# Kernel tuning notes

Measured on AMD Instinct MI355X. Metric: run time of the kernel, lower is better.

Reference implementation:

```python
import jax, jax.numpy as jnp
import numpy as np

HID = 128
N_BATCH = 16384


def gru_cell(x, h, Wih, Whh, bih, bhh):
    # PyTorch GRUCell: weight_ih [3H, in], weight_hh [3H, H], gate order r,z,n
    gi = x @ Wih.T + bih            # [N, 3H]
    gh = h @ Whh.T + bhh            # [N, 3H]
    ir, iz, ic = jnp.split(gi, 3, axis=-1)
    hr, hz, hc = jnp.split(gh, 3, axis=-1)
    r = jax.nn.sigmoid(ir + hr)
    z = jax.nn.sigmoid(iz + hz)
    c = jnp.tanh(ic + r * hc)
    return (1.0 - z) * c + z * h


def setup_inputs() -> dict:
    key = jax.random.key(0)
    ks = jax.random.split(key, 11)
    s = 0.05  # small init like uniform(-1/sqrt(H), 1/sqrt(H))
    return {
        "x": jax.random.normal(ks[0], (N_BATCH, 1, 28, 28), jnp.float32),
        "Wih1": jax.random.normal(ks[1], (3 * HID, 28), jnp.float32) * s,
        "Whh1": jax.random.normal(ks[2], (3 * HID, HID), jnp.float32) * s,
        "bih1": jax.random.normal(ks[3], (3 * HID,), jnp.float32) * s,
        "bhh1": jax.random.normal(ks[4], (3 * HID,), jnp.float32) * s,
        "Wih2": jax.random.normal(ks[5], (3 * HID, HID), jnp.float32) * s,
        "Whh2": jax.random.normal(ks[6], (3 * HID, HID), jnp.float32) * s,
        "bih2": jax.random.normal(ks[7], (3 * HID,), jnp.float32) * s,
        "bhh2": jax.random.normal(ks[8], (3 * HID,), jnp.float32) * s,
        "Wout": jax.random.normal(ks[9], (10, HID), jnp.float32) * s,
        "bout": jax.random.normal(ks[10], (10,), jnp.float32) * s,
    }


def reference(x, Wih1, Whh1, bih1, bhh1, Wih2, Whh2, bih2, bhh2, Wout, bout):
    n, c, h, w = x.shape
    xs = x.transpose(0, 2, 1, 3).reshape(n, h, w * c)  # [N, T=28, 28]
    xs = jnp.swapaxes(xs, 0, 1)                        # [T, N, 28]
    h1_0 = jnp.zeros((n, HID), x.dtype)
    zeros_h = jnp.zeros((n, HID), x.dtype)  # cell2 gets a fresh zero hidden each step (bug in source, kept)

    def step(h1, xt):
        h0 = jax.nn.relu(gru_cell(xt, h1, Wih1, Whh1, bih1, bhh1))
        h1_new = gru_cell(h0, zeros_h, Wih2, Whh2, bih2, bhh2)
        return h1_new, None

    h1, _ = jax.lax.scan(step, h1_0, xs)
    return h1 @ Wout.T + bout  # [N, 10]
```

## Files before the change

### kernel.cpp

```cpp
#include <hip/hip_runtime.h>
#include <hip/hip_bf16.h>
#include <stdint.h>

#define HID 128
#define NB 16384
#define TSTEPS 28
#define BN 64

typedef __attribute__((ext_vector_type(8))) short s16x8;
typedef __attribute__((ext_vector_type(4))) float f32x4;

#define H1_OFF 0
#define H0_OFF 17408
#define XT_OFF 34816
#define WI2_OFF 45056
#define SMEM_BYTES 143360
#define HSTRIDE 272
#define RFSTRIDE 4352
#define XSTRIDE 80

#define L2E 1.442695041f
#define TL2E 2.885390082f

__device__ __forceinline__ unsigned cvtpk2(float lo, float hi) {
  unsigned r;
  asm("v_cvt_pk_bf16_f32 %0, %1, %2" : "=v"(r) : "v"(lo), "v"(hi));
  return r;
}
__device__ __forceinline__ float sig_pre(float acc, float nb) {
  float e = __builtin_amdgcn_exp2f(fmaf(acc, -L2E, nb));
  return __builtin_amdgcn_rcpf(1.0f + e);
}
__device__ __forceinline__ float tanh_nc(float x) {
  float e2 = __builtin_amdgcn_exp2f(x * TL2E);
  float q = __builtin_amdgcn_rcpf(1.0f + e2);
  return fmaf(-2.0f, q, 1.0f);
}

__global__ __launch_bounds__(1024, 1) void gru_kernel(
    const float* __restrict__ x,
    const float* __restrict__ Wih1, const float* __restrict__ Whh1,
    const float* __restrict__ bih1, const float* __restrict__ bhh1,
    const float* __restrict__ Wih2,
    const float* __restrict__ bih2, const float* __restrict__ bhh2,
    const float* __restrict__ Wout, const float* __restrict__ bout,
    float* __restrict__ out)
{
  __shared__ char smem[SMEM_BYTES];
  const int tid = threadIdx.x;
  const int wv16 = tid >> 6;
  const int mh   = wv16 >> 3;
  const int cw   = wv16 & 7;
  const int lane = tid & 63;
  const int l15 = lane & 15;
  const int l16 = lane >> 4;
  const int hc0 = cw * 16;
  const int n0 = blockIdx.x * BN;

  f32x4 zq = {0.f, 0.f, 0.f, 0.f};
  asm("" : "+v"(zq));

  const int hrd = (mh * 32 + l15) * HSTRIDE + l16 * 16;
  const int hwr = (mh * 32 + 4 * l16) * HSTRIDE + (hc0 + l15) * 2;
  const int srow = tid >> 4, skp = tid & 15;
  const int xrd = XT_OFF + (mh * 32 + l15) * XSTRIDE + l16 * 16;
  const int xwr = XT_OFF + srow * XSTRIDE + skp * 4;
  const int wib = WI2_OFF + cw * 12288 + lane * 16;

  s16x8 fw_hh1[4][3];
  s16x8 fw_ih1[3];
  const int gb0 = hc0, gb1 = 128 + hc0, gb2 = 256 + hc0;
  #pragma unroll
  for (int kf = 0; kf < 4; ++kf) {
    int kbase = kf * 32 + l16 * 8;
    #pragma unroll
    for (int cb = 0; cb < 3; ++cb) {
      int g = (cb == 0 ? gb0 : cb == 1 ? gb1 : gb2) + l15;
      const float* p1 = Whh1 + g * HID + kbase;
      s16x8 f1;
      #pragma unroll
      for (int j = 0; j < 8; j += 2) {
        unsigned u1 = cvtpk2(p1[j], p1[j + 1]);
        f1[j] = (short)u1; f1[j + 1] = (short)(u1 >> 16);
      }
      fw_hh1[kf][cb] = f1;
      if (mh == 0) {
        const float* p2 = Wih2 + g * HID + kbase;
        s16x8 f2;
        #pragma unroll
        for (int j = 0; j < 8; j += 2) {
          unsigned u2 = cvtpk2(p2[j], p2[j + 1]);
          f2[j] = (short)u2; f2[j + 1] = (short)(u2 >> 16);
        }
        *(s16x8*)(smem + wib + (kf * 3 + cb) * 1024) = f2;
      }
    }
  }
  {
    int kbase = l16 * 8;
    #pragma unroll
    for (int cb = 0; cb < 3; ++cb) {
      int g = (cb == 0 ? gb0 : cb == 1 ? gb1 : gb2) + l15;
      s16x8 f;
      #pragma unroll
      for (int j = 0; j < 8; ++j) {
        int k = kbase + j;
        f[j] = (k < 28) ? (short)cvtpk2(Wih1[g * 28 + k], 0.f) : (short)0;
      }
      fw_ih1[cb] = f;
    }
  }
  const float nb_r  = -L2E * (bih1[gb0 + l15] + bhh1[gb0 + l15]);
  const float nb_z  = -L2E * (bih1[gb1 + l15] + bhh1[gb1 + l15]);
  const float b_ci  = bih1[gb2 + l15];
  const float b_ch  = bhh1[gb2 + l15];
  const float nb_r2 = -L2E * (bih2[gb0 + l15] + bhh2[gb0 + l15]);
  const float nb_z2 = -L2E * (bih2[gb1 + l15] + bhh2[gb1 + l15]);
  const float c_c2  = bih2[gb2 + l15];
  const float c_hc2 = bhh2[gb2 + l15];

  float h1reg[2][4];
  #pragma unroll
  for (int rf = 0; rf < 2; ++rf)
    #pragma unroll
    for (int j = 0; j < 4; ++j) h1reg[rf][j] = 0.f;

  const float2* xp0 = (const float2*)(x + (size_t)(n0 + srow) * 784 + 2 * skp);

  {
    float2 v0 = make_float2(0.f, 0.f);
    if (skp < 14) v0 = *xp0;
    xp0 += 14;
    *(unsigned*)(smem + xwr) = cvtpk2(v0.x, v0.y);
  }
  ((int4*)(smem + H1_OFF))[tid] = make_int4(0, 0, 0, 0);
  if (tid < 64) ((int4*)(smem + H1_OFF))[tid + 1024] = make_int4(0, 0, 0, 0);
  __syncthreads();

  #pragma unroll 1
  for (int t = 0; t < TSTEPS; ++t) {
    const int xb = (t & 1) * 5120;
    #pragma unroll
    for (int rf = 0; rf < 2; ++rf) {
      s16x8 ax = *(const s16x8*)(smem + xrd + xb + rf * 1280);
      f32x4 aR, aZ, aCi, aCh;
      aR  = __builtin_amdgcn_mfma_f32_16x16x32_bf16(ax, fw_ih1[0], zq, 0, 0, 0);
      aZ  = __builtin_amdgcn_mfma_f32_16x16x32_bf16(ax, fw_ih1[1], zq, 0, 0, 0);
      aCi = __builtin_amdgcn_mfma_f32_16x16x32_bf16(ax, fw_ih1[2], zq, 0, 0, 0);
      #pragma unroll
      for (int kf = 0; kf < 4; ++kf) {
        s16x8 ah = *(const s16x8*)(smem + H1_OFF + hrd + rf * RFSTRIDE + kf * 64);
        aR = __builtin_amdgcn_mfma_f32_16x16x32_bf16(ah, fw_hh1[kf][0], aR, 0, 0, 0);
        aZ = __builtin_amdgcn_mfma_f32_16x16x32_bf16(ah, fw_hh1[kf][1], aZ, 0, 0, 0);
        aCh = (kf == 0)
            ? __builtin_amdgcn_mfma_f32_16x16x32_bf16(ah, fw_hh1[0][2], zq, 0, 0, 0)
            : __builtin_amdgcn_mfma_f32_16x16x32_bf16(ah, fw_hh1[kf][2], aCh, 0, 0, 0);
      }
      float h0v[4];
      #pragma unroll
      for (int j = 0; j < 4; ++j) {
        float r = sig_pre(aR[j], nb_r);
        float z = sig_pre(aZ[j], nb_z);
        float c = tanh_nc(fmaf(r, aCh[j] + b_ch, aCi[j] + b_ci));
        h0v[j] = fmaxf(fmaf(z, h1reg[rf][j] - c, c), 0.f);
      }
      unsigned pk01 = cvtpk2(h0v[0], h0v[1]);
      unsigned pk23 = cvtpk2(h0v[2], h0v[3]);
      *(short*)(smem + H0_OFF + hwr + rf * RFSTRIDE + 0 * HSTRIDE) = (short)pk01;
      *(short*)(smem + H0_OFF + hwr + rf * RFSTRIDE + 1 * HSTRIDE) = (short)(pk01 >> 16);
      *(short*)(smem + H0_OFF + hwr + rf * RFSTRIDE + 2 * HSTRIDE) = (short)pk23;
      *(short*)(smem + H0_OFF + hwr + rf * RFSTRIDE + 3 * HSTRIDE) = (short)(pk23 >> 16);
    }
    __syncthreads();

    float2 xv0 = make_float2(0.f, 0.f);
    const bool do_stage = (t + 1 < TSTEPS);
    if (do_stage && skp < 14) xv0 = *xp0;
    xp0 += 14;
    #pragma unroll
    for (int p = 0; p < 2; ++p) {
      f32x4 aR2, aZ2, aC2;
      #pragma unroll
      for (int kf = 0; kf < 4; ++kf) {
        s16x8 a0 = *(const s16x8*)(smem + H0_OFF + hrd + p * RFSTRIDE + kf * 64);
        s16x8 b0 = *(const s16x8*)(smem + wib + (kf * 3 + 0) * 1024);
        s16x8 b1 = *(const s16x8*)(smem + wib + (kf * 3 + 1) * 1024);
        s16x8 b2 = *(const s16x8*)(smem + wib + (kf * 3 + 2) * 1024);
        if (kf == 0) {
          aR2 = __builtin_amdgcn_mfma_f32_16x16x32_bf16(a0, b0, zq, 0, 0, 0);
          aZ2 = __builtin_amdgcn_mfma_f32_16x16x32_bf16(a0, b1, zq, 0, 0, 0);
          aC2 = __builtin_amdgcn_mfma_f32_16x16x32_bf16(a0, b2, zq, 0, 0, 0);
        } else {
          aR2 = __builtin_amdgcn_mfma_f32_16x16x32_bf16(a0, b0, aR2, 0, 0, 0);
          aZ2 = __builtin_amdgcn_mfma_f32_16x16x32_bf16(a0, b1, aZ2, 0, 0, 0);
          aC2 = __builtin_amdgcn_mfma_f32_16x16x32_bf16(a0, b2, aC2, 0, 0, 0);
        }
      }
      float hv[4];
      #pragma unroll
      for (int j = 0; j < 4; ++j) {
        float r2 = sig_pre(aR2[j], nb_r2);
        float z2 = sig_pre(aZ2[j], nb_z2);
        float c2 = tanh_nc(fmaf(r2, c_hc2, aC2[j] + c_c2));
        float h1n = fmaf(-z2, c2, c2);
        h1reg[p][j] = h1n;
        hv[j] = h1n;
      }
      unsigned pk01 = cvtpk2(hv[0], hv[1]);
      unsigned pk23 = cvtpk2(hv[2], hv[3]);
      *(short*)(smem + H1_OFF + hwr + p * RFSTRIDE + 0 * HSTRIDE) = (short)pk01;
      *(short*)(smem + H1_OFF + hwr + p * RFSTRIDE + 1 * HSTRIDE) = (short)(pk01 >> 16);
      *(short*)(smem + H1_OFF + hwr + p * RFSTRIDE + 2 * HSTRIDE) = (short)pk23;
      *(short*)(smem + H1_OFF + hwr + p * RFSTRIDE + 3 * HSTRIDE) = (short)(pk23 >> 16);
    }
    if (do_stage) {
      const int xo = 5120 - xb;
      *(unsigned*)(smem + xwr + xo) = cvtpk2(xv0.x, xv0.y);
    }
    __syncthreads();
  }

  float* houtf = (float*)smem;
  #pragma unroll
  for (int rf = 0; rf < 2; ++rf)
    #pragma unroll
    for (int j = 0; j < 4; ++j) {
      int row = mh * 32 + rf * 16 + l16 * 4 + j;
      houtf[row * 132 + hc0 + l15] = h1reg[rf][j];
    }
  __syncthreads();
  if (tid < BN * 10) {
    int row = tid & 63;
    int o = tid >> 6;
    const float* hp = houtf + row * 132;
    const float* wp = Wout + o * HID;
    float s = bout[o];
    #pragma unroll 8
    for (int j2 = 0; j2 < HID; ++j2) s = fmaf(hp[j2], wp[j2], s);
    out[(size_t)(n0 + row) * 10 + o] = s;
  }
}

extern "C" void kernel_launch(void* const* d_in, const int* in_sizes, int n_in,
                              void* d_out, int out_size, void* d_ws, size_t ws_size,
                              hipStream_t stream) {
  const float* x    = (const float*)d_in[0];
  const float* Wih1 = (const float*)d_in[1];
  const float* Whh1 = (const float*)d_in[2];
  const float* bih1 = (const float*)d_in[3];
  const float* bhh1 = (const float*)d_in[4];
  const float* Wih2 = (const float*)d_in[5];
  const float* bih2 = (const float*)d_in[7];
  const float* bhh2 = (const float*)d_in[8];
  const float* Wout = (const float*)d_in[9];
  const float* bout = (const float*)d_in[10];
  gru_kernel<<<NB / BN, 1024, 0, stream>>>(x, Wih1, Whh1, bih1, bhh1,
                                           Wih2, bih2, bhh2, Wout, bout,
                                           (float*)d_out);
}
```

Before: 148.0 us.

## Halve block size, move Wih2 fragments to global workspace via prep kernel

```diff
diff --git a/kernel.cpp b/kernel.cpp
--- a/kernel.cpp
+++ b/kernel.cpp
@@ -5,16 +5,15 @@
 #define HID 128
 #define NB 16384
 #define TSTEPS 28
-#define BN 64
+#define BN 32
 
 typedef __attribute__((ext_vector_type(8))) short s16x8;
 typedef __attribute__((ext_vector_type(4))) float f32x4;
 
 #define H1_OFF 0
-#define H0_OFF 17408
-#define XT_OFF 34816
-#define WI2_OFF 45056
-#define SMEM_BYTES 143360
+#define H0_OFF 8704
+#define XT_OFF 17408
+#define SMEM_BYTES 22528
 #define HSTRIDE 272
 #define RFSTRIDE 4352
 #define XSTRIDE 80
@@ -37,20 +36,33 @@
   return fmaf(-2.0f, q, 1.0f);
 }
 
-__global__ __launch_bounds__(1024, 1) void gru_kernel(
+__global__ void prep_wih2(const float* __restrict__ Wih2, char* __restrict__ ws) {
+  const int b = blockIdx.x;
+  const int lane = threadIdx.x;
+  const int cb = b % 3, kf = (b / 3) & 3, cw = b / 12;
+  const int g = cb * 128 + cw * 16 + (lane & 15);
+  const float* p = Wih2 + g * HID + kf * 32 + (lane >> 4) * 8;
+  s16x8 f;
+  #pragma unroll
+  for (int j = 0; j < 8; j += 2) {
+    unsigned u = cvtpk2(p[j], p[j + 1]);
+    f[j] = (short)u; f[j + 1] = (short)(u >> 16);
+  }
+  *(s16x8*)(ws + (b * 64 + lane) * 16) = f;
+}
+
+__global__ __launch_bounds__(512, 4) void gru_kernel(
     const float* __restrict__ x,
     const float* __restrict__ Wih1, const float* __restrict__ Whh1,
     const float* __restrict__ bih1, const float* __restrict__ bhh1,
-    const float* __restrict__ Wih2,
+    const char* __restrict__ wfrag,
     const float* __restrict__ bih2, const float* __restrict__ bhh2,
     const float* __restrict__ Wout, const float* __restrict__ bout,
     float* __restrict__ out)
 {
   __shared__ char smem[SMEM_BYTES];
   const int tid = threadIdx.x;
-  const int wv16 = tid >> 6;
-  const int mh   = wv16 >> 3;
-  const int cw   = wv16 & 7;
+  const int cw   = tid >> 6;
   const int lane = tid & 63;
   const int l15 = lane & 15;
   const int l16 = lane >> 4;
@@ -60,12 +72,12 @@
   f32x4 zq = {0.f, 0.f, 0.f, 0.f};
   asm("" : "+v"(zq));
 
-  const int hrd = (mh * 32 + l15) * HSTRIDE + l16 * 16;
-  const int hwr = (mh * 32 + 4 * l16) * HSTRIDE + (hc0 + l15) * 2;
+  const int hrd = l15 * HSTRIDE + l16 * 16;
+  const int hwr = (4 * l16) * HSTRIDE + (hc0 + l15) * 2;
   const int srow = tid >> 4, skp = tid & 15;
-  const int xrd = XT_OFF + (mh * 32 + l15) * XSTRIDE + l16 * 16;
+  const int xrd = XT_OFF + l15 * XSTRIDE + l16 * 16;
   const int xwr = XT_OFF + srow * XSTRIDE + skp * 4;
-  const int wib = WI2_OFF + cw * 12288 + lane * 16;
+  const char* wsb = wfrag + cw * 12288 + lane * 16;
 
   s16x8 fw_hh1[4][3];
   s16x8 fw_ih1[3];
@@ -84,16 +96,6 @@
         f1[j] = (short)u1; f1[j + 1] = (short)(u1 >> 16);
       }
       fw_hh1[kf][cb] = f1;
-      if (mh == 0) {
-        const float* p2 = Wih2 + g * HID + kbase;
-        s16x8 f2;
-        #pragma unroll
-        for (int j = 0; j < 8; j += 2) {
-          unsigned u2 = cvtpk2(p2[j], p2[j + 1]);
-          f2[j] = (short)u2; f2[j + 1] = (short)(u2 >> 16);
-        }
-        *(s16x8*)(smem + wib + (kf * 3 + cb) * 1024) = f2;
-      }
     }
   }
   {
@@ -134,12 +136,12 @@
     *(unsigned*)(smem + xwr) = cvtpk2(v0.x, v0.y);
   }
   ((int4*)(smem + H1_OFF))[tid] = make_int4(0, 0, 0, 0);
-  if (tid < 64) ((int4*)(smem + H1_OFF))[tid + 1024] = make_int4(0, 0, 0, 0);
+  if (tid < 32) ((int4*)(smem + H1_OFF))[tid + 512] = make_int4(0, 0, 0, 0);
   __syncthreads();
 
   #pragma unroll 1
   for (int t = 0; t < TSTEPS; ++t) {
-    const int xb = (t & 1) * 5120;
+    const int xb = (t & 1) * 2560;
     #pragma unroll
     for (int rf = 0; rf < 2; ++rf) {
       s16x8 ax = *(const s16x8*)(smem + xrd + xb + rf * 1280);
@@ -177,44 +179,60 @@
     const bool do_stage = (t + 1 < TSTEPS);
     if (do_stage && skp < 14) xv0 = *xp0;
     xp0 += 14;
-    #pragma unroll
-    for (int p = 0; p < 2; ++p) {
-      f32x4 aR2, aZ2, aC2;
+    {
+      f32x4 aR2[2], aZ2[2], aC2[2];
+      s16x8 b0a = *(const s16x8*)(wsb + 0);
+      s16x8 b1a = *(const s16x8*)(wsb + 1024);
+      s16x8 b2a = *(const s16x8*)(wsb + 2048);
       #pragma unroll
       for (int kf = 0; kf < 4; ++kf) {
-        s16x8 a0 = *(const s16x8*)(smem + H0_OFF + hrd + p * RFSTRIDE + kf * 64);
-        s16x8 b0 = *(const s16x8*)(smem + wib + (kf * 3 + 0) * 1024);
-        s16x8 b1 = *(const s16x8*)(smem + wib + (kf * 3 + 1) * 1024);
-        s16x8 b2 = *(const s16x8*)(smem + wib + (kf * 3 + 2) * 1024);
+        s16x8 b0n, b1n, b2n;
+        if (kf < 3) {
+          b0n = *(const s16x8*)(wsb + (kf * 3 + 3) * 1024);
+          b1n = *(const s16x8*)(wsb + (kf * 3 + 4) * 1024);
+          b2n = *(const s16x8*)(wsb + (kf * 3 + 5) * 1024);
+        }
+        s16x8 a0 = *(const s16x8*)(smem + H0_OFF + hrd + kf * 64);
+        s16x8 a1 = *(const s16x8*)(smem + H0_OFF + hrd + RFSTRIDE + kf * 64);
         if (kf == 0) {
-          aR2 = __builtin_amdgcn_mfma_f32_16x16x32_bf16(a0, b0, zq, 0, 0, 0);
-          aZ2 = __builtin_amdgcn_mfma_f32_16x16x32_bf16(a0, b1, zq, 0, 0, 0);
-          aC2 = __builtin_amdgcn_mfma_f32_16x16x32_bf16(a0, b2, zq, 0, 0, 0);
+          aR2[0] = __builtin_amdgcn_mfma_f32_16x16x32_bf16(a0, b0a, zq, 0, 0, 0);
+          aR2[1] = __builtin_amdgcn_mfma_f32_16x16x32_bf16(a1, b0a, zq, 0, 0, 0);
+          aZ2[0] = __builtin_amdgcn_mfma_f32_16x16x32_bf16(a0, b1a, zq, 0, 0, 0);
+          aZ2[1] = __builtin_amdgcn_mfma_f32_16x16x32_bf16(a1, b1a, zq, 0, 0, 0);
+          aC2[0] = __builtin_amdgcn_mfma_f32_16x16x32_bf16(a0, b2a, zq, 0, 0, 0);
+          aC2[1] = __builtin_amdgcn_mfma_f32_16x16x32_bf16(a1, b2a, zq, 0, 0, 0);
         } else {
-          aR2 = __builtin_amdgcn_mfma_f32_16x16x32_bf16(a0, b0, aR2, 0, 0, 0);
-          aZ2 = __builtin_amdgcn_mfma_f32_16x16x32_bf16(a0, b1, aZ2, 0, 0, 0);
-          aC2 = __builtin_amdgcn_mfma_f32_16x16x32_bf16(a0, b2, aC2, 0, 0, 0);
+          aR2[0] = __builtin_amdgcn_mfma_f32_16x16x32_bf16(a0, b0a, aR2[0], 0, 0, 0);
+          aR2[1] = __builtin_amdgcn_mfma_f32_16x16x32_bf16(a1, b0a, aR2[1], 0, 0, 0);
+          aZ2[0] = __builtin_amdgcn_mfma_f32_16x16x32_bf16(a0, b1a, aZ2[0], 0, 0, 0);
+          aZ2[1] = __builtin_amdgcn_mfma_f32_16x16x32_bf16(a1, b1a, aZ2[1], 0, 0, 0);
+          aC2[0] = __builtin_amdgcn_mfma_f32_16x16x32_bf16(a0, b2a, aC2[0], 0, 0, 0);
+          aC2[1] = __builtin_amdgcn_mfma_f32_16x16x32_bf16(a1, b2a, aC2[1], 0, 0, 0);
         }
-      }
-      float hv[4];
-      #pragma unroll
-      for (int j = 0; j < 4; ++j) {
-        float r2 = sig_pre(aR2[j], nb_r2);
-        float z2 = sig_pre(aZ2[j], nb_z2);
-        float c2 = tanh_nc(fmaf(r2, c_hc2, aC2[j] + c_c2));
-        float h1n = fmaf(-z2, c2, c2);
-        h1reg[p][j] = h1n;
-        hv[j] = h1n;
-      }
-      unsigned pk01 = cvtpk2(hv[0], hv[1]);
-      unsigned pk23 = cvtpk2(hv[2], hv[3]);
-      *(short*)(smem + H1_OFF + hwr + p * RFSTRIDE + 0 * HSTRIDE) = (short)pk01;
-      *(short*)(smem + H1_OFF + hwr + p * RFSTRIDE + 1 * HSTRIDE) = (short)(pk01 >> 16);
-      *(short*)(smem + H1_OFF + hwr + p * RFSTRIDE + 2 * HSTRIDE) = (short)pk23;
-      *(short*)(smem + H1_OFF + hwr + p * RFSTRIDE + 3 * HSTRIDE) = (short)(pk23 >> 16);
+        b0a = b0n; b1a = b1n; b2a = b2n;
+      }
+      #pragma unroll
+      for (int p = 0; p < 2; ++p) {
+        float hv[4];
+        #pragma unroll
+        for (int j = 0; j < 4; ++j) {
+          float r2 = sig_pre(aR2[p][j], nb_r2);
+          float z2 = sig_pre(aZ2[p][j], nb_z2);
+          float c2 = tanh_nc(fmaf(r2, c_hc2, aC2[p][j] + c_c2));
+          float h1n = fmaf(-z2, c2, c2);
+          h1reg[p][j] = h1n;
+          hv[j] = h1n;
+        }
+        unsigned pk01 = cvtpk2(hv[0], hv[1]);
+        unsigned pk23 = cvtpk2(hv[2], hv[3]);
+        *(short*)(smem + H1_OFF + hwr + p * RFSTRIDE + 0 * HSTRIDE) = (short)pk01;
+        *(short*)(smem + H1_OFF + hwr + p * RFSTRIDE + 1 * HSTRIDE) = (short)(pk01 >> 16);
+        *(short*)(smem + H1_OFF + hwr + p * RFSTRIDE + 2 * HSTRIDE) = (short)pk23;
+        *(short*)(smem + H1_OFF + hwr + p * RFSTRIDE + 3 * HSTRIDE) = (short)(pk23 >> 16);
+      }
     }
     if (do_stage) {
-      const int xo = 5120 - xb;
+      const int xo = 2560 - xb;
       *(unsigned*)(smem + xwr + xo) = cvtpk2(xv0.x, xv0.y);
     }
     __syncthreads();
@@ -225,13 +243,13 @@
   for (int rf = 0; rf < 2; ++rf)
     #pragma unroll
     for (int j = 0; j < 4; ++j) {
-      int row = mh * 32 + rf * 16 + l16 * 4 + j;
+      int row = rf * 16 + l16 * 4 + j;
       houtf[row * 132 + hc0 + l15] = h1reg[rf][j];
     }
   __syncthreads();
   if (tid < BN * 10) {
-    int row = tid & 63;
-    int o = tid >> 6;
+    int row = tid & 31;
+    int o = tid >> 5;
     const float* hp = houtf + row * 132;
     const float* wp = Wout + o * HID;
     float s = bout[o];
@@ -254,7 +272,9 @@
   const float* bhh2 = (const float*)d_in[8];
   const float* Wout = (const float*)d_in[9];
   const float* bout = (const float*)d_in[10];
-  gru_kernel<<<NB / BN, 1024, 0, stream>>>(x, Wih1, Whh1, bih1, bhh1,
-                                           Wih2, bih2, bhh2, Wout, bout,
-                                           (float*)d_out);
-}
+  char* ws = (char*)d_ws;
+  prep_wih2<<<96, 64, 0, stream>>>(Wih2, ws);
+  gru_kernel<<<NB / BN, 512, 0, stream>>>(x, Wih1, Whh1, bih1, bhh1,
+                                          ws, bih2, bhh2, Wout, bout,
+                                          (float*)d_out);
+}
```

Result: slower. 176.9 us (+19.5%).
